# Kernel tuning notes

Hardware: AMD Instinct MI355X
Metric: run time of the kernel (lower is better)

Reference implementation:

```python
import jax, jax.numpy as jnp
import numpy as np

N_NODES = 50000
N_EDGES = 1600000
D_IN = 512
D_OUT = 512


def setup_inputs() -> dict:
    key = jax.random.key(0)
    k1, k2, k3, k4, k5 = jax.random.split(key, 5)
    inputs = jax.random.normal(k1, (N_NODES, D_IN), dtype=jnp.float32)
    # xavier_uniform for weight [D_IN, D_OUT]
    limit = float(np.sqrt(6.0 / (D_IN + D_OUT)))
    weight = jax.random.uniform(k2, (D_IN, D_OUT), dtype=jnp.float32, minval=-limit, maxval=limit)
    adj_rows = jnp.sort(jax.random.randint(k3, (N_EDGES,), 0, N_NODES, dtype=jnp.int32))
    adj_cols = jax.random.randint(k4, (N_EDGES,), 0, N_NODES, dtype=jnp.int32)
    adj_vals = jax.random.uniform(k5, (N_EDGES,), dtype=jnp.float32)
    return {"inputs": inputs, "weight": weight, "adj_rows": adj_rows,
            "adj_cols": adj_cols, "adj_vals": adj_vals}


def reference(inputs, weight, adj_rows, adj_cols, adj_vals):
    # dropout(p=0.0) is identity in this configuration
    support = inputs @ weight                      # [N, D_OUT] dense GEMM
    gathered = support[adj_cols] * adj_vals[:, None]   # [E, D_OUT]
    output = jax.ops.segment_sum(gathered, adj_rows, num_segments=N_NODES)  # spmm
    return output
```

## Files before the change

kernel.cpp:

```cpp
#include <hip/hip_runtime.h>
#include <hip/hip_bf16.h>

#define N_NODES 50000
#define N_EDGES 1600000
#define D 512

typedef __attribute__((ext_vector_type(8))) short short8;
typedef __attribute__((ext_vector_type(4))) float f32x4;
typedef __attribute__((ext_vector_type(2))) float f32x2;
typedef __attribute__((ext_vector_type(8))) unsigned short u16x8;

__device__ __forceinline__ void async_copy16(const void* g, void* l) {
    __builtin_amdgcn_global_load_lds(
        (const __attribute__((address_space(1))) unsigned int*)g,
        (__attribute__((address_space(3))) unsigned int*)l, 16, 0, 0);
}

__global__ __launch_bounds__(256) void cvt_kernel(const float* __restrict__ X,
                                                  unsigned short* __restrict__ Xb) {
    size_t idx = (size_t)(blockIdx.x * 256 + threadIdx.x) * 8;
    f32x4 v0 = *(const f32x4*)(X + idx);
    f32x4 v1 = *(const f32x4*)(X + idx + 4);
    u16x8 u;
#pragma unroll
    for (int k = 0; k < 4; ++k) {
        u[k]     = __bfloat16_as_ushort(__float2bfloat16(v0[k]));
        u[k + 4] = __bfloat16_as_ushort(__float2bfloat16(v1[k]));
    }
    *(u16x8*)(Xb + idx) = u;
}

__global__ __launch_bounds__(256) void wt_kernel(const float* __restrict__ W,
                                                 unsigned short* __restrict__ Wt) {
    int idx = blockIdx.x * 256 + threadIdx.x;
    int k = idx >> 9;
    int n = idx & 511;
    Wt[n * D + k] = __bfloat16_as_ushort(__float2bfloat16(W[k * D + n]));
}

__global__ __launch_bounds__(256) void rowptr_kernel(const int* __restrict__ rows,
                                                     int* __restrict__ row_start) {
    int r = blockIdx.x * 256 + threadIdx.x;
    if (r > N_NODES) return;
    int lo = 0, hi = N_EDGES;
    while (lo < hi) {
        int mid = (lo + hi) >> 1;
        if (rows[mid] < r) lo = mid + 1; else hi = mid;
    }
    row_start[r] = lo;
}

__global__ __launch_bounds__(256) void gemm_kernel(const unsigned short* __restrict__ Xb,
                                                   const unsigned short* __restrict__ Wt,
                                                   __hip_bfloat16* __restrict__ support) {
    __shared__ unsigned short As[128 * 32];
    __shared__ unsigned short Bs[128 * 32];

    const int t = threadIdx.x;
    const int lane = t & 63;
    const int wave = t >> 6;
    const int wm = (wave & 1) * 64;
    const int wn = (wave >> 1) * 64;
    const int m0 = blockIdx.x * 128;
    const int n0 = blockIdx.y * 128;
    const int l15 = lane & 15;
    const int quad = lane >> 4;

    f32x4 acc[4][4];
#pragma unroll
    for (int i = 0; i < 4; ++i)
#pragma unroll
        for (int j = 0; j < 4; ++j) acc[i][j] = (f32x4)(0.0f);

    const int srow = t >> 2;
    const int skb = (t & 3) * 8;
    int gra = m0 + srow;        if (gra > N_NODES - 1) gra = N_NODES - 1;
    int grb = m0 + 64 + srow;   if (grb > N_NODES - 1) grb = N_NODES - 1;
    const size_t aoff0 = (size_t)gra * D + skb;
    const size_t aoff1 = (size_t)grb * D + skb;
    const size_t boff0 = (size_t)(n0 + srow) * D + skb;
    const size_t boff1 = (size_t)(n0 + 64 + srow) * D + skb;
    unsigned short* lA = As + t * 8;
    unsigned short* lB = Bs + t * 8;

    for (int kt = 0; kt < D / 32; ++kt) {
        const int k0 = kt * 32;
        async_copy16(Xb + aoff0 + k0, lA);
        async_copy16(Xb + aoff1 + k0, lA + 2048);
        async_copy16(Wt + boff0 + k0, lB);
        async_copy16(Wt + boff1 + k0, lB + 2048);
        __syncthreads();

        short8 af[4], bf[4];
#pragma unroll
        for (int i = 0; i < 4; ++i) af[i] = *(const short8*)(As + (wm + i * 16 + l15) * 32 + quad * 8);
#pragma unroll
        for (int j = 0; j < 4; ++j) bf[j] = *(const short8*)(Bs + (wn + j * 16 + l15) * 32 + quad * 8);
#pragma unroll
        for (int i = 0; i < 4; ++i)
#pragma unroll
            for (int j = 0; j < 4; ++j)
                acc[i][j] = __builtin_amdgcn_mfma_f32_16x16x32_bf16(af[i], bf[j], acc[i][j], 0, 0, 0);
        __syncthreads();
    }

#pragma unroll
    for (int i = 0; i < 4; ++i) {
        int grow = m0 + wm + i * 16 + quad * 4;
#pragma unroll
        for (int j = 0; j < 4; ++j) {
            int gc = n0 + wn + j * 16 + l15;
#pragma unroll
            for (int rr = 0; rr < 4; ++rr) {
                int gr = grow + rr;
                if (gr < N_NODES)
                    support[(size_t)gr * D + gc] = __float2bfloat16(acc[i][j][rr]);
            }
        }
    }
}

__global__ __launch_bounds__(256) void spmm_kernel(const unsigned short* __restrict__ support,
                                                   const int* __restrict__ cols,
                                                   const float* __restrict__ vals,
                                                   const int* __restrict__ row_start,
                                                   float* __restrict__ out) {
    const int r = blockIdx.x;
    const int t = threadIdx.x;
    const int s = row_start[r];
    const int e = row_start[r + 1];
    const size_t co = 2 * t;

    float ax = 0.f, ay = 0.f;
    int i = s;
    for (; i + 8 <= e; i += 8) {
        int c[8]; float v[8]; unsigned int h[8];
#pragma unroll
        for (int k = 0; k < 8; ++k) { c[k] = cols[i + k]; v[k] = vals[i + k]; }
#pragma unroll
        for (int k = 0; k < 8; ++k)
            h[k] = *(const unsigned int*)(support + (size_t)c[k] * D + co);
#pragma unroll
        for (int k = 0; k < 8; ++k) {
            ax += v[k] * __uint_as_float(h[k] << 16);
            ay += v[k] * __uint_as_float(h[k] & 0xffff0000u);
        }
    }
    for (; i < e; ++i) {
        int c = cols[i];
        float v = vals[i];
        unsigned int h = *(const unsigned int*)(support + (size_t)c * D + co);
        ax += v * __uint_as_float(h << 16);
        ay += v * __uint_as_float(h & 0xffff0000u);
    }
    f32x2 o; o[0] = ax; o[1] = ay;
    __builtin_nontemporal_store(o, (f32x2*)(out + (size_t)r * D + co));
}

extern "C" void kernel_launch(void* const* d_in, const int* in_sizes, int n_in,
                              void* d_out, int out_size, void* d_ws, size_t ws_size,
                              hipStream_t stream) {
    (void)in_sizes; (void)n_in; (void)out_size; (void)ws_size;
    const float* X    = (const float*)d_in[0];
    const float* W    = (const float*)d_in[1];
    const int* rows   = (const int*)d_in[2];
    const int* cols   = (const int*)d_in[3];
    const float* vals = (const float*)d_in[4];
    float* out = (float*)d_out;

    unsigned short* support = (unsigned short*)d_ws;
    unsigned short* Wt      = support + (size_t)N_NODES * D;
    int* row_start          = (int*)(Wt + (size_t)D * D);
    unsigned short* Xb = (unsigned short*)d_out;

    cvt_kernel<<<12500, 256, 0, stream>>>(X, Xb);
    wt_kernel<<<(D * D) / 256, 256, 0, stream>>>(W, Wt);
    rowptr_kernel<<<(N_NODES + 256) / 256, 256, 0, stream>>>(rows, row_start);

    dim3 gg((N_NODES + 127) / 128, D / 128);
    gemm_kernel<<<gg, 256, 0, stream>>>(Xb, Wt, (__hip_bfloat16*)support);

    spmm_kernel<<<N_NODES, 256, 0, stream>>>(support, cols, vals, row_start, out);
}
```

Before: 462.1 us.

## Merge prep kernels into one launch and split SpMM into eight row chunks

```diff
diff --git a/kernel.cpp b/kernel.cpp
--- a/kernel.cpp
+++ b/kernel.cpp
@@ -16,38 +16,42 @@
         (__attribute__((address_space(3))) unsigned int*)l, 16, 0, 0);
 }
 
-__global__ __launch_bounds__(256) void cvt_kernel(const float* __restrict__ X,
-                                                  unsigned short* __restrict__ Xb) {
-    size_t idx = (size_t)(blockIdx.x * 256 + threadIdx.x) * 8;
-    f32x4 v0 = *(const f32x4*)(X + idx);
-    f32x4 v1 = *(const f32x4*)(X + idx + 4);
-    u16x8 u;
+#define CVT_BLOCKS 12500
+#define WT_BLOCKS  1024
+#define RP_BLOCKS  196
+__global__ __launch_bounds__(256) void prep_kernel(const float* __restrict__ X,
+                                                   unsigned short* __restrict__ Xb,
+                                                   const float* __restrict__ W,
+                                                   unsigned short* __restrict__ Wt,
+                                                   const int* __restrict__ rows,
+                                                   int* __restrict__ row_start) {
+    const int b = blockIdx.x;
+    if (b < CVT_BLOCKS) {
+        size_t idx = (size_t)(b * 256 + threadIdx.x) * 8;
+        f32x4 v0 = *(const f32x4*)(X + idx);
+        f32x4 v1 = *(const f32x4*)(X + idx + 4);
+        u16x8 u;
 #pragma unroll
-    for (int k = 0; k < 4; ++k) {
-        u[k]     = __bfloat16_as_ushort(__float2bfloat16(v0[k]));
-        u[k + 4] = __bfloat16_as_ushort(__float2bfloat16(v1[k]));
+        for (int k = 0; k < 4; ++k) {
+            u[k]     = __bfloat16_as_ushort(__float2bfloat16(v0[k]));
+            u[k + 4] = __bfloat16_as_ushort(__float2bfloat16(v1[k]));
+        }
+        *(u16x8*)(Xb + idx) = u;
+    } else if (b < CVT_BLOCKS + WT_BLOCKS) {
+        int idx = (b - CVT_BLOCKS) * 256 + threadIdx.x;
+        int k = idx >> 9;
+        int n = idx & 511;
+        Wt[n * D + k] = __bfloat16_as_ushort(__float2bfloat16(W[k * D + n]));
+    } else {
+        int r = (b - CVT_BLOCKS - WT_BLOCKS) * 256 + threadIdx.x;
+        if (r > N_NODES) return;
+        int lo = 0, hi = N_EDGES;
+        while (lo < hi) {
+            int mid = (lo + hi) >> 1;
+            if (rows[mid] < r) lo = mid + 1; else hi = mid;
+        }
+        row_start[r] = lo;
     }
-    *(u16x8*)(Xb + idx) = u;
-}
-
-__global__ __launch_bounds__(256) void wt_kernel(const float* __restrict__ W,
-                                                 unsigned short* __restrict__ Wt) {
-    int idx = blockIdx.x * 256 + threadIdx.x;
-    int k = idx >> 9;
-    int n = idx & 511;
-    Wt[n * D + k] = __bfloat16_as_ushort(__float2bfloat16(W[k * D + n]));
-}
-
-__global__ __launch_bounds__(256) void rowptr_kernel(const int* __restrict__ rows,
-                                                     int* __restrict__ row_start) {
-    int r = blockIdx.x * 256 + threadIdx.x;
-    if (r > N_NODES) return;
-    int lo = 0, hi = N_EDGES;
-    while (lo < hi) {
-        int mid = (lo + hi) >> 1;
-        if (rows[mid] < r) lo = mid + 1; else hi = mid;
-    }
-    row_start[r] = lo;
 }
 
 __global__ __launch_bounds__(256) void gemm_kernel(const unsigned short* __restrict__ Xb,
@@ -124,8 +128,10 @@
                                                    const int* __restrict__ cols,
                                                    const float* __restrict__ vals,
                                                    const int* __restrict__ row_start,
-                                                   float* __restrict__ out) {
-    const int r = blockIdx.x;
+                                                   float* __restrict__ out,
+                                                   int r0) {
+    const int r = r0 + blockIdx.x;
+    if (r >= N_NODES) return;
     const int t = threadIdx.x;
     const int s = row_start[r];
     const int e = row_start[r + 1];
@@ -173,12 +179,12 @@
     int* row_start          = (int*)(Wt + (size_t)D * D);
     unsigned short* Xb = (unsigned short*)d_out;
 
-    cvt_kernel<<<12500, 256, 0, stream>>>(X, Xb);
-    wt_kernel<<<(D * D) / 256, 256, 0, stream>>>(W, Wt);
-    rowptr_kernel<<<(N_NODES + 256) / 256, 256, 0, stream>>>(rows, row_start);
+    prep_kernel<<<CVT_BLOCKS + WT_BLOCKS + RP_BLOCKS, 256, 0, stream>>>(
+        X, Xb, W, Wt, rows, row_start);
 
     dim3 gg((N_NODES + 127) / 128, D / 128);
     gemm_kernel<<<gg, 256, 0, stream>>>(Xb, Wt, (__hip_bfloat16*)support);
 
-    spmm_kernel<<<N_NODES, 256, 0, stream>>>(support, cols, vals, row_start, out);
+    for (int p = 0; p < 8; ++p)
+        spmm_kernel<<<6250, 256, 0, stream>>>(support, cols, vals, row_start, out, p * 6250);
 }
```

New measurement: 490.9 us. 1.06x slower.
